# Optimization experiments

Hardware: AMD Instinct MI355X
Metric: run time of the kernel (lower is better)

## Reference

```python
import jax, jax.numpy as jnp
import numpy as np

EPS = 1e-8  # smoothing_radius


def setup_inputs() -> dict:
    key = jax.random.key(0)
    ks = jax.random.split(key, 8)
    T, S, D = 2048, 1024, 3
    H, FIN, FOUT = 64, 7, 4
    return {
        "reference_length": jnp.ones((), jnp.float32),
        "source_points": jax.random.normal(ks[0], (S, D), jnp.float32),
        "target_points": jax.random.normal(ks[1], (T, D), jnp.float32),
        "source_strengths": jax.random.uniform(ks[2], (S,), jnp.float32),
        "source_area": jax.random.uniform(ks[3], (S,), jnp.float32),
        "source_normal": jax.random.normal(ks[4], (S, D), jnp.float32),
        "W1": jax.random.normal(ks[5], (FIN, H), jnp.float32) / np.sqrt(FIN),
        "b1": jnp.zeros((H,), jnp.float32),
        "W2": jax.random.normal(ks[6], (H, FOUT), jnp.float32) / np.sqrt(H),
        "b2": jnp.zeros((FOUT,), jnp.float32),
    }


def _legendre4(x):
    # First 4 Legendre polynomials P1..P4 (n_spherical_harmonics = 4)
    x2 = x * x
    p1 = x
    p2 = 0.5 * (3.0 * x2 - 1.0)
    p3 = 0.5 * (5.0 * x2 - 3.0) * x
    p4 = 0.125 * ((35.0 * x2 - 30.0) * x2 + 3.0)
    return jnp.stack([p1, p2, p3, p4], axis=-1)


def _kernel_forward(reference_length, source_points, target_points,
                    source_strengths, source_area, source_normal,
                    W1, b1, W2, b2):
    D = source_points.shape[-1]
    # Dimensionless relative positions: [T, S, D]
    r = (target_points[:, None, :] - source_points[None, :, :]) / reference_length
    r2 = jnp.sum(r * r, axis=-1) + EPS * EPS          # [T, S]
    n2 = jnp.sum(source_normal * source_normal, -1) + EPS * EPS  # [S]
    # Invariant features: source scalar, smoothed log-magnitudes, pair Legendre terms
    log_r = 0.5 * jnp.log(r2)                          # [T, S]
    log_n = 0.5 * jnp.log(n2)                          # [S]
    cos = jnp.einsum('tsd,sd->ts', r, source_normal) / jnp.sqrt(r2 * n2[None, :])
    feats = jnp.concatenate([
        jnp.broadcast_to(source_area[None, :, None], r2.shape + (1,)),
        log_r[..., None],
        jnp.broadcast_to(log_n[None, :, None], r2.shape + (1,)),
        _legendre4(cos),
    ], axis=-1)                                        # [T, S, 7]
    # MLP kernel network with tanh squashing (network_type='mlp')
    h = jax.nn.silu(feats @ W1 + b1)                   # [T, S, 64]
    out = jnp.tanh(h @ W2 + b2)                        # [T, S, 4]
    # Physical far-field decay: scalar ~ 1/r^{D-2}, vector ~ 1/r^{D-1}
    inv_r = jax.lax.rsqrt(r2)
    decay_s = inv_r ** (D - 2)
    decay_v = inv_r ** (D - 1)
    w = source_strengths[None, :]                      # [1, S]
    scalar = jnp.sum(w * decay_s * out[..., 0], axis=-1)  # [T]
    # Rotationally invariant vector reprojection: radial + 2 coeffs per non-radial vector
    r_hat = r * inv_r[..., None]
    n_hat = source_normal / jnp.sqrt(n2)[:, None]
    n_hat_b = jnp.broadcast_to(n_hat[None], r.shape)
    vec = (out[..., 1:2] * r_hat
           + out[..., 2:3] * n_hat_b
           + out[..., 3:4] * jnp.cross(r_hat, n_hat_b))  # [T, S, D]
    vector = jnp.einsum('ts,tsd->td', w * decay_v, vec)   # [T, D]
    return jnp.concatenate([scalar[:, None], vector], axis=-1)  # [T, 1+D]


def reference(reference_length, source_points, target_points, source_strengths,
              source_area, source_normal, W1, b1, W2, b2):
    return _kernel_forward(reference_length, source_points, target_points,
                           source_strengths, source_area, source_normal,
                           W1, b1, W2, b2)
```

## Files before the change

### kernel.cpp

```cpp
#include <hip/hip_runtime.h>

typedef float v2f __attribute__((ext_vector_type(2)));

#define EPS2 1e-16f

constexpr int H      = 64;
constexpr int BLOCK  = 256;
constexpr int NCHUNK = 4;
constexpr float HALF_LN2 = 0.34657359027997264f;

__device__ __forceinline__ float rcpf_fast(float x) { return __builtin_amdgcn_rcpf(x); }
__device__ __forceinline__ float rsqf_fast(float x) { return __builtin_amdgcn_rsqf(x); }
__device__ __forceinline__ v2f splat(float x) { return v2f{x, x}; }
__device__ __forceinline__ v2f vfma(v2f a, v2f b, v2f c) { return __builtin_elementwise_fma(a, b, c); }

__global__ void prep(const float* __restrict__ refLenP,
                     const float* __restrict__ srcP,
                     const float* __restrict__ srcN,
                     const float* __restrict__ wgtP,
                     const float* __restrict__ areaP,
                     const float* __restrict__ W1,
                     const float* __restrict__ b1,
                     const float* __restrict__ W2,
                     float* __restrict__ ws, int S)
{
    const int nSrcBlk = (S + BLOCK - 1) / BLOCK;
    const int bid = blockIdx.x;
    if (bid < nSrcBlk) {
        const int s = bid * BLOCK + threadIdx.x;
        if (s < S) {
            const float invL = rcpf_fast(refLenP[0]);
            float px = srcP[s * 3 + 0] * invL;
            float py = srcP[s * 3 + 1] * invL;
            float pz = srcP[s * 3 + 2] * invL;
            float nx = srcN[s * 3 + 0];
            float ny = srcN[s * 3 + 1];
            float nz = srcN[s * 3 + 2];
            float n2 = fmaf(nx, nx, fmaf(ny, ny, nz * nz)) + EPS2;
            float inv_n = rsqf_fast(n2);
            float l2n = __log2f(n2);
            float4* sPA = (float4*)(ws + 1024);
            float4* sNB = (float4*)(ws + 1024 + 4 * S);
            float*  sw  = ws + 1024 + 8 * S;
            sPA[s] = make_float4(px, py, pz, areaP[s]);
            sNB[s] = make_float4(nx * inv_n, ny * inv_n, nz * inv_n, l2n);
            sw[s]  = wgtP[s];
        }
    } else {
        const int h = threadIdx.x;
        if (h < H) {
            float* p = ws + h * 16;
            p[0] = W1[0 * H + h];
            p[1] = W1[1 * H + h] * HALF_LN2;
            p[2] = W1[2 * H + h] * HALF_LN2;
            p[3] = W1[3 * H + h];
            p[4] = W1[4 * H + h];
            p[5] = W1[5 * H + h];
            p[6] = W1[6 * H + h];
            p[7] = b1[h];
            p[8]  = 2.0f * W2[h * 4 + 0];
            p[9]  = 2.0f * W2[h * 4 + 1];
            p[10] = 2.0f * W2[h * 4 + 2];
            p[11] = 2.0f * W2[h * 4 + 3];
            p[12] = 0.f; p[13] = 0.f; p[14] = 0.f; p[15] = 0.f;
        }
    }
}

__global__ __launch_bounds__(BLOCK)
void bh_kernel(const float* __restrict__ refLenP,
               const float* __restrict__ tgtP,
               const float* __restrict__ b2,
               const float* __restrict__ ws,
               float* __restrict__ out,
               int S, int T)
{
    __shared__ float red[4][8];

    const int tid = threadIdx.x;
    const int t0 = blockIdx.x * 2;
    const int t1 = t0 + 1;
    const bool has1 = (t1 < T);
    const int t1c = has1 ? t1 : t0;

    const float invL = rcpf_fast(refLenP[0]);
    const v2f txv = v2f{tgtP[t0 * 3 + 0] * invL, tgtP[t1c * 3 + 0] * invL};
    const v2f tyv = v2f{tgtP[t0 * 3 + 1] * invL, tgtP[t1c * 3 + 1] * invL};
    const v2f tzv = v2f{tgtP[t0 * 3 + 2] * invL, tgtP[t1c * 3 + 2] * invL};

    const float4* __restrict__ sPA = (const float4*)(ws + 1024);
    const float4* __restrict__ sNB = (const float4*)(ws + 1024 + 4 * S);
    const float*  __restrict__ sw  = ws + 1024 + 8 * S;
    const float4* __restrict__ wq  = (const float4*)ws;

    v2f f1[NCHUNK], f3[NCHUNK], f4[NCHUNK], f5[NCHUNK], f6[NCHUNK];
    float fa[NCHUNK], f2s[NCHUNK];
    #pragma unroll
    for (int c = 0; c < NCHUNK; ++c) {
        const int s = tid + c * BLOCK;
        const int sc = (s < S) ? s : (S - 1);
        const float4 pa = sPA[sc];
        const float4 nb = sNB[sc];
        v2f rx = txv - splat(pa.x);
        v2f ry = tyv - splat(pa.y);
        v2f rz = tzv - splat(pa.z);
        v2f r2 = vfma(rx, rx, vfma(ry, ry, vfma(rz, rz, splat(EPS2))));
        v2f ir = v2f{rsqf_fast(r2.x), rsqf_fast(r2.y)};
        f1[c] = v2f{__log2f(r2.x), __log2f(r2.y)};
        v2f cosv = vfma(rx, splat(nb.x), vfma(ry, splat(nb.y), rz * splat(nb.z))) * ir;
        v2f c2 = cosv * cosv;
        fa[c]  = pa.w;
        f2s[c] = nb.w;
        f3[c] = cosv;
        f4[c] = vfma(c2, splat(1.5f), splat(-0.5f));
        f5[c] = (c2 * splat(2.5f) - splat(1.5f)) * cosv;
        f6[c] = vfma(vfma(c2, splat(4.375f), splat(-3.75f)), c2, splat(0.375f));
    }

    v2f o0[NCHUNK], o1[NCHUNK], o2[NCHUNK], o3[NCHUNK];
    {
        const float b20 = 2.0f * b2[0], b21 = 2.0f * b2[1];
        const float b22 = 2.0f * b2[2], b23 = 2.0f * b2[3];
        #pragma unroll
        for (int c = 0; c < NCHUNK; ++c) {
            o0[c] = splat(b20); o1[c] = splat(b21);
            o2[c] = splat(b22); o3[c] = splat(b23);
        }
    }

    #pragma unroll 2
    for (int h = 0; h < H; ++h) {
        const float4 wa = wq[h * 4 + 0];
        const float4 wb = wq[h * 4 + 1];
        const float4 w2 = wq[h * 4 + 2];
        #pragma unroll
        for (int c = 0; c < NCHUNK; ++c) {
            float abase = fmaf(fa[c], wa.x, fmaf(f2s[c], wa.z, wb.w));
            v2f a = vfma(f1[c], splat(wa.y), splat(abase));
            a = vfma(f3[c], splat(wa.w), a);
            a = vfma(f4[c], splat(wb.x), a);
            a = vfma(f5[c], splat(wb.y), a);
            a = vfma(f6[c], splat(wb.z), a);
            v2f e  = v2f{__expf(-a.x), __expf(-a.y)};
            v2f sg = v2f{rcpf_fast(1.0f + e.x), rcpf_fast(1.0f + e.y)};
            v2f hv = a * sg;
            o0[c] = vfma(hv, splat(w2.x), o0[c]);
            o1[c] = vfma(hv, splat(w2.y), o1[c]);
            o2[c] = vfma(hv, splat(w2.z), o2[c]);
            o3[c] = vfma(hv, splat(w2.w), o3[c]);
        }
    }

    v2f a0 = splat(0.f), a1 = splat(0.f), a2 = splat(0.f), a3 = splat(0.f);
    #pragma unroll
    for (int c = 0; c < NCHUNK; ++c) {
        const int s = tid + c * BLOCK;
        const int sc = (s < S) ? s : (S - 1);
        const float4 pa = sPA[sc];
        const float4 nb = sNB[sc];
        const float wgt = (s < S) ? sw[sc] : 0.0f;
        v2f rx = txv - splat(pa.x);
        v2f ry = tyv - splat(pa.y);
        v2f rz = tzv - splat(pa.z);
        v2f r2 = vfma(rx, rx, vfma(ry, ry, vfma(rz, rz, splat(EPS2))));
        v2f ir = v2f{rsqf_fast(r2.x), rsqf_fast(r2.y)};
        v2f wsv = splat(wgt) * ir;
        v2f wvv = wsv * ir;

        v2f tt[4];
        v2f oo[4] = {o0[c], o1[c], o2[c], o3[c]};
        #pragma unroll
        for (int k = 0; k < 4; ++k) {
            v2f m = __builtin_elementwise_min(__builtin_elementwise_max(oo[k], splat(-80.f)), splat(80.f));
            v2f e = v2f{__expf(m.x), __expf(m.y)};
            v2f num = e - splat(1.0f);
            v2f den = v2f{rcpf_fast(e.x + 1.0f), rcpf_fast(e.y + 1.0f)};
            tt[k] = num * den;
        }

        a0 = vfma(wsv, tt[0], a0);
        v2f rhx = rx * ir, rhy = ry * ir, rhz = rz * ir;
        v2f cxx = rhy * splat(nb.z) - rhz * splat(nb.y);
        v2f cxy = rhz * splat(nb.x) - rhx * splat(nb.z);
        v2f cxz = rhx * splat(nb.y) - rhy * splat(nb.x);
        v2f vx = tt[1] * rhx + tt[2] * splat(nb.x) + tt[3] * cxx;
        v2f vy = tt[1] * rhy + tt[2] * splat(nb.y) + tt[3] * cxy;
        v2f vz = tt[1] * rhz + tt[2] * splat(nb.z) + tt[3] * cxz;
        a1 = vfma(wvv, vx, a1);
        a2 = vfma(wvv, vy, a2);
        a3 = vfma(wvv, vz, a3);
    }

    float r8[8] = {a0.x, a1.x, a2.x, a3.x, a0.y, a1.y, a2.y, a3.y};
    #pragma unroll
    for (int off = 32; off > 0; off >>= 1) {
        #pragma unroll
        for (int k = 0; k < 8; ++k) r8[k] += __shfl_down(r8[k], off);
    }
    const int wave = tid >> 6;
    const int lane = tid & 63;
    if (lane == 0) {
        #pragma unroll
        for (int k = 0; k < 8; ++k) red[wave][k] = r8[k];
    }
    __syncthreads();
    if (tid < 8) {
        float v = red[0][tid] + red[1][tid] + red[2][tid] + red[3][tid];
        if (tid < 4) out[t0 * 4 + tid] = v;
        else if (has1) out[t1 * 4 + (tid - 4)] = v;
    }
}

extern "C" void kernel_launch(void* const* d_in, const int* in_sizes, int n_in,
                              void* d_out, int out_size, void* d_ws, size_t ws_size,
                              hipStream_t stream) {
    const float* refLen = (const float*)d_in[0];
    const float* srcP   = (const float*)d_in[1];
    const float* tgtP   = (const float*)d_in[2];
    const float* w      = (const float*)d_in[3];
    const float* area   = (const float*)d_in[4];
    const float* srcN   = (const float*)d_in[5];
    const float* W1     = (const float*)d_in[6];
    const float* b1     = (const float*)d_in[7];
    const float* W2     = (const float*)d_in[8];
    const float* b2     = (const float*)d_in[9];
    float* out          = (float*)d_out;
    float* ws           = (float*)d_ws;

    const int S = in_sizes[3];
    const int T = in_sizes[2] / 3;
    const int nSrcBlk = (S + BLOCK - 1) / BLOCK;
    const int nTgtBlk = (T + 1) / 2;

    prep<<<nSrcBlk + 1, BLOCK, 0, stream>>>(refLen, srcP, srcN, w, area, W1, b1, W2, ws, S);
    bh_kernel<<<nTgtBlk, BLOCK, 0, stream>>>(refLen, tgtP, b2, ws, out, S, T);
}
```

Measured before the change: 124.8 us.

## Fold log2e scaling into MLP weights, use exp2, and widen block to 512

```diff
diff --git a/kernel.cpp b/kernel.cpp
--- a/kernel.cpp
+++ b/kernel.cpp
@@ -5,12 +5,14 @@
 #define EPS2 1e-16f
 
 constexpr int H      = 64;
-constexpr int BLOCK  = 256;
-constexpr int NCHUNK = 4;
-constexpr float HALF_LN2 = 0.34657359027997264f;
+constexpr int PBLOCK = 256;
+constexpr int BLOCK  = 512;
+constexpr int NCHUNK = 2;
+constexpr float LOG2E = 1.4426950408889634f;
 
 __device__ __forceinline__ float rcpf_fast(float x) { return __builtin_amdgcn_rcpf(x); }
 __device__ __forceinline__ float rsqf_fast(float x) { return __builtin_amdgcn_rsqf(x); }
+__device__ __forceinline__ float exp2_fast(float x) { return __builtin_amdgcn_exp2f(x); }
 __device__ __forceinline__ v2f splat(float x) { return v2f{x, x}; }
 __device__ __forceinline__ v2f vfma(v2f a, v2f b, v2f c) { return __builtin_elementwise_fma(a, b, c); }
 
@@ -24,10 +26,10 @@
                      const float* __restrict__ W2,
                      float* __restrict__ ws, int S)
 {
-    const int nSrcBlk = (S + BLOCK - 1) / BLOCK;
+    const int nSrcBlk = (S + PBLOCK - 1) / PBLOCK;
     const int bid = blockIdx.x;
     if (bid < nSrcBlk) {
-        const int s = bid * BLOCK + threadIdx.x;
+        const int s = bid * PBLOCK + threadIdx.x;
         if (s < S) {
             const float invL = rcpf_fast(refLenP[0]);
             float px = srcP[s * 3 + 0] * invL;
@@ -50,24 +52,24 @@
         const int h = threadIdx.x;
         if (h < H) {
             float* p = ws + h * 16;
-            p[0] = W1[0 * H + h];
-            p[1] = W1[1 * H + h] * HALF_LN2;
-            p[2] = W1[2 * H + h] * HALF_LN2;
-            p[3] = W1[3 * H + h];
-            p[4] = W1[4 * H + h];
-            p[5] = W1[5 * H + h];
-            p[6] = W1[6 * H + h];
-            p[7] = b1[h];
-            p[8]  = 2.0f * W2[h * 4 + 0];
-            p[9]  = 2.0f * W2[h * 4 + 1];
-            p[10] = 2.0f * W2[h * 4 + 2];
-            p[11] = 2.0f * W2[h * 4 + 3];
+            p[0] = -LOG2E * W1[0 * H + h];
+            p[1] = -0.5f  * W1[1 * H + h];
+            p[2] = -0.5f  * W1[2 * H + h];
+            p[3] = -LOG2E * W1[3 * H + h];
+            p[4] = -LOG2E * W1[4 * H + h];
+            p[5] = -LOG2E * W1[5 * H + h];
+            p[6] = -LOG2E * W1[6 * H + h];
+            p[7] = -LOG2E * b1[h];
+            p[8]  = -2.0f * W2[h * 4 + 0];
+            p[9]  = -2.0f * W2[h * 4 + 1];
+            p[10] = -2.0f * W2[h * 4 + 2];
+            p[11] = -2.0f * W2[h * 4 + 3];
             p[12] = 0.f; p[13] = 0.f; p[14] = 0.f; p[15] = 0.f;
         }
     }
 }
 
-__global__ __launch_bounds__(BLOCK)
+__global__ __launch_bounds__(BLOCK, 8)
 void bh_kernel(const float* __restrict__ refLenP,
                const float* __restrict__ tgtP,
                const float* __restrict__ b2,
@@ -75,7 +77,7 @@
                float* __restrict__ out,
                int S, int T)
 {
-    __shared__ float red[4][8];
+    __shared__ float red[8][8];
 
     const int tid = threadIdx.x;
     const int t0 = blockIdx.x * 2;
@@ -119,8 +121,9 @@
 
     v2f o0[NCHUNK], o1[NCHUNK], o2[NCHUNK], o3[NCHUNK];
     {
-        const float b20 = 2.0f * b2[0], b21 = 2.0f * b2[1];
-        const float b22 = 2.0f * b2[2], b23 = 2.0f * b2[3];
+        const float s2 = 2.0f * LOG2E;
+        const float b20 = s2 * b2[0], b21 = s2 * b2[1];
+        const float b22 = s2 * b2[2], b23 = s2 * b2[3];
         #pragma unroll
         for (int c = 0; c < NCHUNK; ++c) {
             o0[c] = splat(b20); o1[c] = splat(b21);
@@ -128,7 +131,7 @@
         }
     }
 
-    #pragma unroll 2
+    #pragma unroll 4
     for (int h = 0; h < H; ++h) {
         const float4 wa = wq[h * 4 + 0];
         const float4 wb = wq[h * 4 + 1];
@@ -141,7 +144,7 @@
             a = vfma(f4[c], splat(wb.x), a);
             a = vfma(f5[c], splat(wb.y), a);
             a = vfma(f6[c], splat(wb.z), a);
-            v2f e  = v2f{__expf(-a.x), __expf(-a.y)};
+            v2f e  = v2f{exp2_fast(a.x), exp2_fast(a.y)};
             v2f sg = v2f{rcpf_fast(1.0f + e.x), rcpf_fast(1.0f + e.y)};
             v2f hv = a * sg;
             o0[c] = vfma(hv, splat(w2.x), o0[c]);
@@ -171,10 +174,10 @@
         v2f oo[4] = {o0[c], o1[c], o2[c], o3[c]};
         #pragma unroll
         for (int k = 0; k < 4; ++k) {
-            v2f m = __builtin_elementwise_min(__builtin_elementwise_max(oo[k], splat(-80.f)), splat(80.f));
-            v2f e = v2f{__expf(m.x), __expf(m.y)};
-            v2f num = e - splat(1.0f);
-            v2f den = v2f{rcpf_fast(e.x + 1.0f), rcpf_fast(e.y + 1.0f)};
+            v2f m = __builtin_elementwise_min(__builtin_elementwise_max(oo[k], splat(-126.f)), splat(126.f));
+            v2f E = v2f{exp2_fast(m.x), exp2_fast(m.y)};
+            v2f num = E - splat(1.0f);
+            v2f den = v2f{rcpf_fast(E.x + 1.0f), rcpf_fast(E.y + 1.0f)};
             tt[k] = num * den;
         }
 
@@ -205,7 +208,9 @@
     }
     __syncthreads();
     if (tid < 8) {
-        float v = red[0][tid] + red[1][tid] + red[2][tid] + red[3][tid];
+        float v = 0.0f;
+        #pragma unroll
+        for (int w = 0; w < 8; ++w) v += red[w][tid];
         if (tid < 4) out[t0 * 4 + tid] = v;
         else if (has1) out[t1 * 4 + (tid - 4)] = v;
     }
@@ -229,9 +234,9 @@
 
     const int S = in_sizes[3];
     const int T = in_sizes[2] / 3;
-    const int nSrcBlk = (S + BLOCK - 1) / BLOCK;
+    const int nSrcBlk = (S + PBLOCK - 1) / PBLOCK;
     const int nTgtBlk = (T + 1) / 2;
 
-    prep<<<nSrcBlk + 1, BLOCK, 0, stream>>>(refLen, srcP, srcN, w, area, W1, b1, W2, ws, S);
+    prep<<<nSrcBlk + 1, PBLOCK, 0, stream>>>(refLen, srcP, srcN, w, area, W1, b1, W2, ws, S);
     bh_kernel<<<nTgtBlk, BLOCK, 0, stream>>>(refLen, tgtP, b2, ws, out, S, T);
 }
```

Result: faster. 120.5 us (-3.4%).
